# Performance work log

Hardware: AMD Instinct MI355X
Metric: run time of the kernel (lower is better)

## Reference

```python
import jax, jax.numpy as jnp
import numpy as np

N = 100000
E = 600000
IN_DIM = 128
OUT_DIM = 256
BN_EPS = 1e-5


def setup_inputs() -> dict:
    key = jax.random.key(0)
    ks = jax.random.split(key, 12)
    x = jax.random.normal(ks[0], (N, IN_DIM), dtype=jnp.float32)
    edge_index = jax.random.randint(ks[1], (2, E), 0, N, dtype=jnp.int64)
    s1 = 1.0 / np.sqrt(IN_DIM)
    s2 = 1.0 / np.sqrt(OUT_DIM)
    return {
        "x": x,
        "edge_index": edge_index,
        "eps": jnp.zeros((), dtype=jnp.float32),  # GINConv eps init = 0
        "W1": jax.random.uniform(ks[2], (IN_DIM, OUT_DIM), jnp.float32, -s1, s1),
        "b1": jnp.zeros((OUT_DIM,), jnp.float32),
        "W2": jax.random.uniform(ks[3], (OUT_DIM, OUT_DIM), jnp.float32, -s2, s2),
        "b2": jnp.zeros((OUT_DIM,), jnp.float32),
        "gamma": jnp.ones((OUT_DIM,), jnp.float32),
        "beta": jnp.zeros((OUT_DIM,), jnp.float32),
        "run_mean": jnp.zeros((OUT_DIM,), jnp.float32),
        "run_var": jnp.ones((OUT_DIM,), jnp.float32),
        "Wp": jax.random.uniform(ks[4], (IN_DIM, OUT_DIM), jnp.float32, -s1, s1),
        "bp": jnp.zeros((OUT_DIM,), jnp.float32),
    }


def reference(x, edge_index, eps, W1, b1, W2, b2, gamma, beta, run_mean, run_var, Wp, bp):
    src, dst = edge_index[0], edge_index[1]
    # GIN aggregation: sum_{j in N(i)} x_j  (scatter-add of source features to dst)
    agg = jax.ops.segment_sum(x[src], dst, num_segments=N)
    h = (1.0 + eps) * x + agg            # [N, in_dim]
    # 2-layer MLP (nn1)
    h = jax.nn.relu(h @ W1 + b1) @ W2 + b2   # [N, out_dim]
    # BatchNorm1d (eval mode: running stats); dropout = identity (eval)
    h = (h - run_mean) * jax.lax.rsqrt(run_var + BN_EPS) * gamma + beta
    # residual with projection (in_dim != out_dim)
    return h + x @ Wp + bp
```

## Files before the change

### kernel.cpp

```cpp
#include <hip/hip_runtime.h>

#define N_ 100000
#define E_ 600000
#define IND_ 128
#define OUTD_ 256
#define NT_ (N_/16)
#define NB_ 98
#define CASTN_ (N_*IND_/2)

typedef __attribute__((ext_vector_type(8))) short bf16x8;
typedef __attribute__((ext_vector_type(4))) float f32x4;
typedef __attribute__((ext_vector_type(2))) unsigned int u32x2;

static __device__ __forceinline__ unsigned f2bf_u(float f){
  union { float f; unsigned u; } v; v.f = f;
  return (v.u + 0x7fffu + ((v.u >> 16) & 1u)) >> 16;
}
static __device__ __forceinline__ unsigned pack2(float a, float b){
  return f2bf_u(a) | (f2bf_u(b) << 16);
}
static __device__ __forceinline__ float blo(unsigned u){
  union { unsigned u; float f; } v; v.u = u << 16; return v.f;
}
static __device__ __forceinline__ float bhi(unsigned u){
  union { unsigned u; float f; } v; v.u = u & 0xffff0000u; return v.f;
}
static __device__ __forceinline__ void gload_lds16(const bf16x8* g, bf16x8* l){
  __builtin_amdgcn_global_load_lds((const __attribute__((address_space(1))) void*)g,
                                   (__attribute__((address_space(3))) void*)l, 16, 0, 0);
}

__global__ void k_prep(const float* __restrict__ x,
                       const float* __restrict__ W1, const float* __restrict__ W2,
                       const float* __restrict__ Wp, const float* __restrict__ b2,
                       const float* __restrict__ gamma, const float* __restrict__ beta,
                       const float* __restrict__ mean, const float* __restrict__ var,
                       const float* __restrict__ bp,
                       const int* __restrict__ dst, int* __restrict__ deg,
                       unsigned short* __restrict__ W1s, unsigned short* __restrict__ W2s,
                       unsigned short* __restrict__ Wps,
                       float* __restrict__ scale, float* __restrict__ shift,
                       unsigned* __restrict__ xbw)
{
  int gid = blockIdx.x*256 + threadIdx.x;
  if (gid < 16384) {
    const float* W; unsigned short* Ws; int u;
    if (gid < 4096)       { W = W1; Ws = W1s; u = gid; }
    else if (gid < 12288) { W = W2; Ws = W2s; u = gid - 4096; }
    else                  { W = Wp; Ws = Wps; u = gid - 12288; }
    int l  = u & 63;
    int km = (u >> 6) & 1;
    int t  = (u >> 7) & 15;
    int q  = u >> 11;
    int kk = 2*q + km;
    int kb = kk*32 + (l >> 4)*8;
    int c  = 16*t + (l & 15);
    #pragma unroll
    for (int j = 0; j < 8; j++)
      Ws[u*8 + j] = (unsigned short)f2bf_u(W[(size_t)(kb + j)*OUTD_ + c]);
  } else if (gid < 16640) {
    int c = gid - 16384;
    float s = gamma[c] * rsqrtf(var[c] + 1e-5f);
    scale[c] = s;
    shift[c] = (b2[c] - mean[c]) * s + beta[c] + bp[c];
  } else if (gid < 16640 + CASTN_) {
    int ci = gid - 16640;
    float2 v = ((const float2*)x)[ci];
    xbw[ci] = pack2(v.x, v.y);
  } else if (gid < 16640 + CASTN_ + E_) {
    int e = gid - 16640 - CASTN_;
    atomicAdd(&deg[dst[e]], 1);
  }
}

__global__ __launch_bounds__(1024) void k_scan1(const int* __restrict__ deg,
                                                int* __restrict__ bsum, int* __restrict__ offs){
  __shared__ int red[16];
  int tid = threadIdx.x;
  int i = blockIdx.x*1024 + tid;
  int v = (i < N_) ? deg[i] : 0;
  #pragma unroll
  for (int d = 32; d; d >>= 1) v += __shfl_down(v, d);
  if ((tid & 63) == 0) red[tid >> 6] = v;
  __syncthreads();
  if (tid < 16) {
    int s = red[tid];
    #pragma unroll
    for (int d = 8; d; d >>= 1) s += __shfl_down(s, d, 16);
    if (tid == 0) bsum[blockIdx.x] = s;
  }
  if (blockIdx.x == 0 && tid == 0) offs[N_] = E_;
}

__global__ __launch_bounds__(1024) void k_scan2(const int* __restrict__ deg,
                                                const int* __restrict__ bsum, int* __restrict__ offs){
  __shared__ int bs[128];
  __shared__ int d1[1024];
  int tid = threadIdx.x;
  if (tid < 128) bs[tid] = (tid < NB_) ? bsum[tid] : 0;
  __syncthreads();
  #pragma unroll
  for (int d = 1; d < 128; d <<= 1){
    int v = (tid < 128 && tid >= d) ? bs[tid - d] : 0;
    __syncthreads();
    if (tid < 128) bs[tid] += v;
    __syncthreads();
  }
  int bprefix = (blockIdx.x > 0) ? bs[blockIdx.x - 1] : 0;
  int i = blockIdx.x*1024 + tid;
  int v = (i < N_) ? deg[i] : 0;
  d1[tid] = v;
  __syncthreads();
  #pragma unroll
  for (int d = 1; d < 1024; d <<= 1){
    int t = (tid >= d) ? d1[tid - d] : 0;
    __syncthreads();
    d1[tid] += t;
    __syncthreads();
  }
  if (i < N_) offs[i] = bprefix + d1[tid] - v;
}

__global__ void k_fill(const int* __restrict__ src, const int* __restrict__ dst,
                       const int* __restrict__ offs, int* __restrict__ cur, int* __restrict__ adj){
  int e = blockIdx.x*256 + threadIdx.x;
  if (e < E_) {
    int d = dst[e];
    int p = atomicAdd(&cur[d], 1);
    adj[offs[d] + p] = src[e];
  }
}

__global__ void k_agg(const unsigned* __restrict__ xb32, const int* __restrict__ offs,
                      const int* __restrict__ adj, const float* __restrict__ epsp,
                      unsigned* __restrict__ h0)
{
  int pair = blockIdx.x*4 + (threadIdx.x >> 6);
  int lane = threadIdx.x & 63;
  int row0 = pair*2;
  if (row0 >= N_) return;
  int b0 = offs[row0], e0 = offs[row0+1], e1 = offs[row0+2];
  int d0 = e0 - b0;
  int total = e1 - b0;
  float a0x0=0,a0y0=0,a0x1=0,a0y1=0,a0x2=0,a0y2=0,a0x3=0,a0y3=0;
  float a1x0=0,a1y0=0,a1x1=0,a1y1=0,a1x2=0,a1y2=0,a1x3=0,a1y3=0;

#define ACC(P, V, S)                                                        \
  { if ((P) < d0) { a0x##S += blo(V); a0y##S += bhi(V); }                   \
    else          { a1x##S += blo(V); a1y##S += bhi(V); } }

  for (int base = 0; base < total; base += 64){
    int cnt = min(64, total - base);
    int idx = adj[b0 + base + min(lane, cnt - 1)];
    int j = 0;
    for (; j + 8 <= cnt; j += 8){
      int n0=__shfl(idx,j+0), n1=__shfl(idx,j+1), n2=__shfl(idx,j+2), n3=__shfl(idx,j+3);
      int n4=__shfl(idx,j+4), n5=__shfl(idx,j+5), n6=__shfl(idx,j+6), n7=__shfl(idx,j+7);
      unsigned v0 = xb32[(size_t)n0*64 + lane];
      unsigned v1 = xb32[(size_t)n1*64 + lane];
      unsigned v2 = xb32[(size_t)n2*64 + lane];
      unsigned v3 = xb32[(size_t)n3*64 + lane];
      unsigned v4 = xb32[(size_t)n4*64 + lane];
      unsigned v5 = xb32[(size_t)n5*64 + lane];
      unsigned v6 = xb32[(size_t)n6*64 + lane];
      unsigned v7 = xb32[(size_t)n7*64 + lane];
      ACC(base+j+0, v0, 0) ACC(base+j+1, v1, 1) ACC(base+j+2, v2, 2) ACC(base+j+3, v3, 3)
      ACC(base+j+4, v4, 0) ACC(base+j+5, v5, 1) ACC(base+j+6, v6, 2) ACC(base+j+7, v7, 3)
    }
    for (; j + 4 <= cnt; j += 4){
      int n0=__shfl(idx,j+0), n1=__shfl(idx,j+1), n2=__shfl(idx,j+2), n3=__shfl(idx,j+3);
      unsigned v0 = xb32[(size_t)n0*64 + lane];
      unsigned v1 = xb32[(size_t)n1*64 + lane];
      unsigned v2 = xb32[(size_t)n2*64 + lane];
      unsigned v3 = xb32[(size_t)n3*64 + lane];
      ACC(base+j+0, v0, 0) ACC(base+j+1, v1, 1) ACC(base+j+2, v2, 2) ACC(base+j+3, v3, 3)
    }
    if (j + 2 <= cnt){
      int n0=__shfl(idx,j+0), n1=__shfl(idx,j+1);
      unsigned v0 = xb32[(size_t)n0*64 + lane];
      unsigned v1 = xb32[(size_t)n1*64 + lane];
      ACC(base+j+0, v0, 0) ACC(base+j+1, v1, 1)
      j += 2;
    }
    if (j < cnt){
      int n = __shfl(idx, j);
      unsigned v = xb32[(size_t)n*64 + lane];
      ACC(base+j, v, 2)
    }
  }
#undef ACC

  float k1 = 1.f + epsp[0];
  unsigned xw0 = xb32[(size_t)row0*64 + lane];
  unsigned xw1 = xb32[(size_t)(row0+1)*64 + lane];
  float a0x = (a0x0 + a0x1) + (a0x2 + a0x3);
  float a0y = (a0y0 + a0y1) + (a0y2 + a0y3);
  float a1x = (a1x0 + a1x1) + (a1x2 + a1x3);
  float a1y = (a1y0 + a1y1) + (a1y2 + a1y3);
  h0[(size_t)row0*64 + lane]     = pack2(fmaf(k1, blo(xw0), a0x), fmaf(k1, bhi(xw0), a0y));
  h0[(size_t)(row0+1)*64 + lane] = pack2(fmaf(k1, blo(xw1), a1x), fmaf(k1, bhi(xw1), a1y));
}

__global__ __launch_bounds__(256, 2) void k_mlp(const unsigned short* __restrict__ h0,
        const unsigned short* __restrict__ xb16,
        const bf16x8* __restrict__ W1s, const float* __restrict__ b1,
        const bf16x8* __restrict__ W2s, const bf16x8* __restrict__ Wps,
        const float* __restrict__ scale, const float* __restrict__ shift,
        float* __restrict__ out)
{
  __shared__ bf16x8 w[4][1024];
  __shared__ __align__(16) char trans[4][2][1280];
  int tid = threadIdx.x;
  int wv = tid >> 6, lane = tid & 63, g = lane >> 4, r = lane & 15;
  int tA0 = blockIdx.x*8 + wv*2;
  int tB0 = tA0 + 1;
  int tA = min(tA0, NT_ - 1);
  int tB = min(tB0, NT_ - 1);

  const bf16x8* hrowA = (const bf16x8*)(h0 + ((size_t)tA*16 + r)*IND_);
  const bf16x8* hrowB = (const bf16x8*)(h0 + ((size_t)tB*16 + r)*IND_);
  bf16x8 BA[4], BB[4];
  #pragma unroll
  for (int kk = 0; kk < 4; kk++) BA[kk] = hrowA[kk*4 + g];
  #pragma unroll
  for (int kk = 0; kk < 4; kk++) BB[kk] = hrowB[kk*4 + g];

  const bf16x8* sl[16];
  #pragma unroll
  for (int i = 0; i < 4; i++)  sl[i]      = W1s + i*1024;
  #pragma unroll
  for (int i = 0; i < 8; i++)  sl[4 + i]  = W2s + i*1024;
  #pragma unroll
  for (int i = 0; i < 4; i++)  sl[12 + i] = Wps + i*1024;

  auto STAGE = [&](int buf, const bf16x8* src){
    #pragma unroll
    for (int i = 0; i < 4; i++)
      gload_lds16(&src[i*256 + wv*64 + lane], &w[buf][i*256 + wv*64]);
  };
  f32x4 accA[16], accB[16];
  auto MF16 = [&](int buf, bf16x8 f0, bf16x8 f1, int tb, f32x4 (&acc)[16]){
    #pragma unroll
    for (int tt = 0; tt < 8; tt++)
      acc[tb+tt] = __builtin_amdgcn_mfma_f32_16x16x32_bf16(w[buf][(tt*2+0)*64 + lane], f0, acc[tb+tt], 0,0,0);
    #pragma unroll
    for (int tt = 0; tt < 8; tt++)
      acc[tb+tt] = __builtin_amdgcn_mfma_f32_16x16x32_bf16(w[buf][(tt*2+1)*64 + lane], f1, acc[tb+tt], 0,0,0);
  };
  #pragma unroll
  for (int t = 0; t < 16; t++){ accA[t] = (f32x4){0.f,0.f,0.f,0.f}; accB[t] = (f32x4){0.f,0.f,0.f,0.f}; }

  const float4* b1v = (const float4*)b1;
  auto EPI = [&](f32x4 (&acc)[16], bf16x8 (&H)[8]){
    #pragma unroll
    for (int kkh = 0; kkh < 8; kkh++){
      char* tr = &trans[wv][kkh & 1][0];
      #pragma unroll
      for (int h = 0; h < 2; h++){
        int t = 2*kkh + h;
        float4 bb = b1v[t*4 + g];
        f32x4 a = acc[t];
        float v0 = fmaxf(a.x + bb.x, 0.f);
        float v1 = fmaxf(a.y + bb.y, 0.f);
        float v2 = fmaxf(a.z + bb.z, 0.f);
        float v3 = fmaxf(a.w + bb.w, 0.f);
        u32x2 dd; dd.x = pack2(v0, v1); dd.y = pack2(v2, v3);
        *(u32x2*)(tr + r*80 + h*32 + g*8) = dd;
      }
      H[kkh] = *(const bf16x8*)(tr + r*80 + g*16);
    }
    #pragma unroll
    for (int t = 0; t < 16; t++) acc[t] = (f32x4){0.f,0.f,0.f,0.f};
  };

#define PHASE(P, VM, FA0, FA1, FB0, FB1, TB)                       \
  { if ((P) + 2 < 16) STAGE(((P)+2)&3, sl[(P)+2]);                 \
    asm volatile("s_waitcnt vmcnt(" VM ")" ::: "memory");          \
    __builtin_amdgcn_s_barrier();                                  \
    __builtin_amdgcn_s_setprio(1);                                 \
    MF16((P)&3, FA0, FA1, TB, accA);                               \
    MF16((P)&3, FB0, FB1, TB, accB);                               \
    __builtin_amdgcn_s_setprio(0); }

  STAGE(0, sl[0]);
  STAGE(1, sl[1]);

  PHASE(0,  "8", BA[0], BA[1], BB[0], BB[1], 0)
  PHASE(1,  "8", BA[0], BA[1], BB[0], BB[1], 8)
  PHASE(2,  "8", BA[2], BA[3], BB[2], BB[3], 0)
  PHASE(3,  "8", BA[2], BA[3], BB[2], BB[3], 8)

  bf16x8 HA[8], HB[8];
  EPI(accA, HA);
  EPI(accB, HB);

  PHASE(4,  "8", HA[0], HA[1], HB[0], HB[1], 0)
  PHASE(5,  "8", HA[0], HA[1], HB[0], HB[1], 8)
  PHASE(6,  "8", HA[2], HA[3], HB[2], HB[3], 0)
  PHASE(7,  "8", HA[2], HA[3], HB[2], HB[3], 8)
  PHASE(8,  "8", HA[4], HA[5], HB[4], HB[5], 0)
  PHASE(9,  "8", HA[4], HA[5], HB[4], HB[5], 8)

  const bf16x8* xrowA = (const bf16x8*)(xb16 + ((size_t)tA*16 + r)*IND_);
  const bf16x8* xrowB = (const bf16x8*)(xb16 + ((size_t)tB*16 + r)*IND_);
  bf16x8 XA[4], XB[4];
  #pragma unroll
  for (int kk = 0; kk < 4; kk++) XA[kk] = xrowA[kk*4 + g];
  #pragma unroll
  for (int kk = 0; kk < 4; kk++) XB[kk] = xrowB[kk*4 + g];

  PHASE(10, "8", HA[6], HA[7], HB[6], HB[7], 0)
  PHASE(11, "8", HA[6], HA[7], HB[6], HB[7], 8)
  PHASE(12, "8", XA[0], XA[1], XB[0], XB[1], 0)
  PHASE(13, "8", XA[0], XA[1], XB[0], XB[1], 8)
  PHASE(14, "4", XA[2], XA[3], XB[2], XB[3], 0)
  PHASE(15, "0", XA[2], XA[3], XB[2], XB[3], 8)
#undef PHASE

  const float4* sc = (const float4*)scale;
  const float4* sh = (const float4*)shift;
  if (tA0 < NT_){
    #pragma unroll
    for (int t = 0; t < 16; t++){
      float4 s = sc[t*4 + g], b = sh[t*4 + g];
      f32x4 a = accA[t];
      float4 o;
      o.x = fmaf(a.x, s.x, b.x);
      o.y = fmaf(a.y, s.y, b.y);
      o.z = fmaf(a.z, s.z, b.z);
      o.w = fmaf(a.w, s.w, b.w);
      *(float4*)(out + ((size_t)tA*16 + r)*OUTD_ + t*16 + g*4) = o;
    }
  }
  if (tB0 < NT_){
    #pragma unroll
    for (int t = 0; t < 16; t++){
      float4 s = sc[t*4 + g], b = sh[t*4 + g];
      f32x4 a = accB[t];
      float4 o;
      o.x = fmaf(a.x, s.x, b.x);
      o.y = fmaf(a.y, s.y, b.y);
      o.z = fmaf(a.z, s.z, b.z);
      o.w = fmaf(a.w, s.w, b.w);
      *(float4*)(out + ((size_t)tB*16 + r)*OUTD_ + t*16 + g*4) = o;
    }
  }
}

extern "C" void kernel_launch(void* const* d_in, const int* in_sizes, int n_in,
                              void* d_out, int out_size, void* d_ws, size_t ws_size,
                              hipStream_t stream)
{
  const float* x     = (const float*)d_in[0];
  const int*   ei    = (const int*)d_in[1];
  const float* eps   = (const float*)d_in[2];
  const float* W1    = (const float*)d_in[3];
  const float* b1    = (const float*)d_in[4];
  const float* W2    = (const float*)d_in[5];
  const float* b2    = (const float*)d_in[6];
  const float* gamma = (const float*)d_in[7];
  const float* beta  = (const float*)d_in[8];
  const float* rmean = (const float*)d_in[9];
  const float* rvar  = (const float*)d_in[10];
  const float* Wp    = (const float*)d_in[11];
  const float* bp    = (const float*)d_in[12];
  float* out = (float*)d_out;

  char* ws = (char*)d_ws; size_t off = 0;
  auto carve = [&](size_t b)->char* { char* p = ws + off; off = (off + b + 255) & ~(size_t)255; return p; };
  unsigned*       xbuf  = (unsigned*)carve((size_t)CASTN_*4);
  unsigned*       h0    = (unsigned*)carve((size_t)N_*64*4);
  unsigned short* W1s   = (unsigned short*)carve(4096*16);
  unsigned short* W2s   = (unsigned short*)carve(8192*16);
  unsigned short* Wps   = (unsigned short*)carve(4096*16);
  float*          scale = (float*)carve(256*4);
  float*          shift = (float*)carve(256*4);
  int*            deg   = (int*)carve((size_t)N_*4);
  int*            cur   = (int*)carve((size_t)N_*4);
  int*            offs  = (int*)carve((size_t)(N_+1)*4);
  int*            adj   = (int*)carve((size_t)E_*4);
  int*            bsum  = (int*)carve((size_t)NB_*4);

  size_t degpad = (((size_t)N_*4 + 255) & ~(size_t)255);
  hipMemsetAsync(deg, 0, degpad + (size_t)N_*4, stream);

  k_prep <<<(16640 + CASTN_ + E_ + 255)/256, 256, 0, stream>>>(x, W1, W2, Wp, b2, gamma, beta,
                                  rmean, rvar, bp, ei + E_, deg,
                                  W1s, W2s, Wps, scale, shift, xbuf);
  k_scan1<<<NB_, 1024, 0, stream>>>(deg, bsum, offs);
  k_scan2<<<NB_, 1024, 0, stream>>>(deg, bsum, offs);
  k_fill <<<(E_+255)/256, 256, 0, stream>>>(ei, ei + E_, offs, cur, adj);
  k_agg  <<<(N_/2+3)/4, 256, 0, stream>>>(xbuf, offs, adj, eps, h0);
  k_mlp  <<<(NT_+7)/8, 256, 0, stream>>>((const unsigned short*)h0, (const unsigned short*)xbuf,
                                         (const bf16x8*)W1s, b1, (const bf16x8*)W2s,
                                         (const bf16x8*)Wps, scale, shift, out);
}
```

Before: 181.4 us.

## Merge two-pass scan into one kernel, widen x cast, drop MFMA setprio

```diff
diff --git a/kernel.cpp b/kernel.cpp
--- a/kernel.cpp
+++ b/kernel.cpp
@@ -7,6 +7,7 @@
 #define NT_ (N_/16)
 #define NB_ 98
 #define CASTN_ (N_*IND_/2)
+#define CAST4_ (CASTN_/2)
 
 typedef __attribute__((ext_vector_type(8))) short bf16x8;
 typedef __attribute__((ext_vector_type(4))) float f32x4;
@@ -63,51 +64,37 @@
     float s = gamma[c] * rsqrtf(var[c] + 1e-5f);
     scale[c] = s;
     shift[c] = (b2[c] - mean[c]) * s + beta[c] + bp[c];
-  } else if (gid < 16640 + CASTN_) {
+  } else if (gid < 16640 + CAST4_) {
     int ci = gid - 16640;
-    float2 v = ((const float2*)x)[ci];
-    xbw[ci] = pack2(v.x, v.y);
-  } else if (gid < 16640 + CASTN_ + E_) {
-    int e = gid - 16640 - CASTN_;
+    float4 v = ((const float4*)x)[ci];
+    u32x2 o; o.x = pack2(v.x, v.y); o.y = pack2(v.z, v.w);
+    ((u32x2*)xbw)[ci] = o;
+  } else if (gid < 16640 + CAST4_ + E_) {
+    int e = gid - 16640 - CAST4_;
     atomicAdd(&deg[dst[e]], 1);
   }
 }
 
-__global__ __launch_bounds__(1024) void k_scan1(const int* __restrict__ deg,
-                                                int* __restrict__ bsum, int* __restrict__ offs){
+__global__ __launch_bounds__(1024) void k_scan(const int* __restrict__ deg, int* __restrict__ offs){
   __shared__ int red[16];
-  int tid = threadIdx.x;
-  int i = blockIdx.x*1024 + tid;
-  int v = (i < N_) ? deg[i] : 0;
-  #pragma unroll
-  for (int d = 32; d; d >>= 1) v += __shfl_down(v, d);
-  if ((tid & 63) == 0) red[tid >> 6] = v;
+  __shared__ int d1[1024];
+  int tid = threadIdx.x, b = blockIdx.x;
+  int s = 0;
+  for (int base = 0; base < b*1024; base += 1024)
+    s += deg[base + tid];
+  #pragma unroll
+  for (int d = 32; d; d >>= 1) s += __shfl_down(s, d);
+  if ((tid & 63) == 0) red[tid >> 6] = s;
   __syncthreads();
   if (tid < 16) {
-    int s = red[tid];
-    #pragma unroll
-    for (int d = 8; d; d >>= 1) s += __shfl_down(s, d, 16);
-    if (tid == 0) bsum[blockIdx.x] = s;
-  }
-  if (blockIdx.x == 0 && tid == 0) offs[N_] = E_;
-}
-
-__global__ __launch_bounds__(1024) void k_scan2(const int* __restrict__ deg,
-                                                const int* __restrict__ bsum, int* __restrict__ offs){
-  __shared__ int bs[128];
-  __shared__ int d1[1024];
-  int tid = threadIdx.x;
-  if (tid < 128) bs[tid] = (tid < NB_) ? bsum[tid] : 0;
+    int t = red[tid];
+    #pragma unroll
+    for (int d = 8; d; d >>= 1) t += __shfl_down(t, d, 16);
+    if (tid == 0) red[0] = t;
+  }
   __syncthreads();
-  #pragma unroll
-  for (int d = 1; d < 128; d <<= 1){
-    int v = (tid < 128 && tid >= d) ? bs[tid - d] : 0;
-    __syncthreads();
-    if (tid < 128) bs[tid] += v;
-    __syncthreads();
-  }
-  int bprefix = (blockIdx.x > 0) ? bs[blockIdx.x - 1] : 0;
-  int i = blockIdx.x*1024 + tid;
+  int bprefix = red[0];
+  int i = b*1024 + tid;
   int v = (i < N_) ? deg[i] : 0;
   d1[tid] = v;
   __syncthreads();
@@ -119,6 +106,7 @@
     __syncthreads();
   }
   if (i < N_) offs[i] = bprefix + d1[tid] - v;
+  if (b == 0 && tid == 0) offs[N_] = E_;
 }
 
 __global__ void k_fill(const int* __restrict__ src, const int* __restrict__ dst,
@@ -277,10 +265,8 @@
   { if ((P) + 2 < 16) STAGE(((P)+2)&3, sl[(P)+2]);                 \
     asm volatile("s_waitcnt vmcnt(" VM ")" ::: "memory");          \
     __builtin_amdgcn_s_barrier();                                  \
-    __builtin_amdgcn_s_setprio(1);                                 \
     MF16((P)&3, FA0, FA1, TB, accA);                               \
-    MF16((P)&3, FB0, FB1, TB, accB);                               \
-    __builtin_amdgcn_s_setprio(0); }
+    MF16((P)&3, FB0, FB1, TB, accB); }
 
   STAGE(0, sl[0]);
   STAGE(1, sl[1]);
@@ -379,16 +365,14 @@
   int*            cur   = (int*)carve((size_t)N_*4);
   int*            offs  = (int*)carve((size_t)(N_+1)*4);
   int*            adj   = (int*)carve((size_t)E_*4);
-  int*            bsum  = (int*)carve((size_t)NB_*4);
 
   size_t degpad = (((size_t)N_*4 + 255) & ~(size_t)255);
   hipMemsetAsync(deg, 0, degpad + (size_t)N_*4, stream);
 
-  k_prep <<<(16640 + CASTN_ + E_ + 255)/256, 256, 0, stream>>>(x, W1, W2, Wp, b2, gamma, beta,
+  k_prep <<<(16640 + CAST4_ + E_ + 255)/256, 256, 0, stream>>>(x, W1, W2, Wp, b2, gamma, beta,
                                   rmean, rvar, bp, ei + E_, deg,
                                   W1s, W2s, Wps, scale, shift, xbuf);
-  k_scan1<<<NB_, 1024, 0, stream>>>(deg, bsum, offs);
-  k_scan2<<<NB_, 1024, 0, stream>>>(deg, bsum, offs);
+  k_scan <<<NB_, 1024, 0, stream>>>(deg, offs);
   k_fill <<<(E_+255)/256, 256, 0, stream>>>(ei, ei + E_, offs, cur, adj);
   k_agg  <<<(N_/2+3)/4, 256, 0, stream>>>(xbuf, offs, adj, eps, h0);
   k_mlp  <<<(NT_+7)/8, 256, 0, stream>>>((const unsigned short*)h0, (const unsigned short*)xbuf,
```

New measurement: 185.3 us. 1.02x slower.
